# Optimization experiments

Measured on AMD Instinct MI355X. Metric: run time of the kernel, lower is better.

The kernel has to match this reference:

```python
import jax, jax.numpy as jnp
import numpy as np

N_VAR, N_CHK, DV, DC = 8192, 4096, 3, 6
N_EDGE = N_VAR * DV  # == N_CHK * DC = 24576
BATCH = 512
N_ITER = 5
EPS = 1e-12
ATANH_CLIP = 1.0 - 1e-7


def setup_inputs() -> dict:
    # Deterministic (3,6)-regular Tanner graph: each variable has DV edges,
    # each check has DC edges; edge-to-check assignment is a fixed permutation.
    rng = np.random.default_rng(0)
    var_index = np.repeat(np.arange(N_VAR, dtype=np.int32), DV)
    chk_index = rng.permutation(np.repeat(np.arange(N_CHK, dtype=np.int32), DC))
    key = jax.random.key(0)
    llr = jax.random.normal(key, (BATCH, N_VAR), dtype=jnp.float32) * 2.0
    return {
        "llr": llr,
        "var_index": jnp.asarray(var_index, jnp.int32),
        "chk_index": jnp.asarray(chk_index, jnp.int32),
    }


def reference(llr, var_index, chk_index):
    # Messages stored edge-major: [E, batch] so segment ops act on leading axis.
    x = llr.T                              # [N, batch]
    scattered = x[var_index]               # spa.scatter(llr) -> [E, batch]
    ext = jnp.zeros_like(scattered)        # extrinsic_value init
    outs = []
    for _ in range(N_ITER):
        # variable node process: leave-one-out sum of check->var extrinsics
        vsum = jax.ops.segment_sum(ext, var_index, num_segments=N_VAR)
        a_priori = vsum[var_index] - ext   # [E, batch]
        msg = a_priori + scattered
        # check node process: 2*atanh( prod_{e' in check, e'!=e} tanh(msg/2) )
        t = jnp.tanh(msg * 0.5)
        log_abs = jnp.log(jnp.abs(t) + EPS)
        sgn = jnp.sign(t)
        csum_log = jax.ops.segment_sum(log_abs, chk_index, num_segments=N_CHK)
        cprod_sgn = jax.ops.segment_prod(sgn, chk_index, num_segments=N_CHK)
        loo = jnp.exp(csum_log[chk_index] - log_abs) * (cprod_sgn[chk_index] * sgn)
        loo = jnp.clip(loo, -ATANH_CLIP, ATANH_CLIP)
        ext = 2.0 * jnp.arctanh(loo)
        # gather(extrinsic) + llr
        out = jax.ops.segment_sum(ext, var_index, num_segments=N_VAR) + x
        outs.append(out.T)                 # back to [batch, N]
    return jnp.stack(outs)                 # [N_ITER, batch, N]
```

## Files before the change

kernel.cpp:

```cpp
#include <hip/hip_runtime.h>
#include <math.h>

#define N_VAR 8192
#define N_CHK 4096
#define DC 6
#define N_EDGE 24576
#define BATCH 512
#define N_ITER 5
#define CLIP_F 0.99999988f
#define NTHREADS 1024
#define VPT (N_VAR / NTHREADS)
#define CPT (N_CHK / NTHREADS)


__global__ void k_zero(int* __restrict__ cnt) {
    int i = blockIdx.x * blockDim.x + threadIdx.x;
    if (i < N_CHK) cnt[i] = 0;
}

__global__ void k_build(const int* __restrict__ chk_index,
                        int* __restrict__ cnt,
                        int* __restrict__ chk_edges) {
    int e = blockIdx.x * blockDim.x + threadIdx.x;
    if (e < N_EDGE) {
        int c = chk_index[e];
        int p = atomicAdd(&cnt[c], 1);
        chk_edges[c * DC + p] = e;
    }
}

__launch_bounds__(1024, 4)
__global__ void k_spa(const float* __restrict__ llr,
                      const int* __restrict__ chk_edges,
                      float* __restrict__ out) {
    __shared__ float m[N_EDGE];
    const int b = blockIdx.x;
    const int tid = threadIdx.x;
    const float* __restrict__ lrow = llr + (size_t)b * N_VAR;
    float* __restrict__ orow = out + (size_t)b * N_VAR;

    float l[VPT], el[VPT];
    #pragma unroll
    for (int k = 0; k < VPT; ++k) {
        int v = tid + k * NTHREADS;
        l[k]  = lrow[v];
        el[k] = __expf(l[k]);
    }
    int ce[CPT][DC];
    #pragma unroll
    for (int k = 0; k < CPT; ++k) {
        int c = tid + k * NTHREADS;
        #pragma unroll
        for (int j = 0; j < DC; ++j) ce[k][j] = chk_edges[c * DC + j];
    }

    #pragma unroll
    for (int k = 0; k < VPT; ++k) {
        int v = tid + k * NTHREADS;
        float t0 = (el[k] - 1.0f) * __builtin_amdgcn_rcpf(el[k] + 1.0f);
        m[3 * v] = t0; m[3 * v + 1] = t0; m[3 * v + 2] = t0;
    }
    __syncthreads();

    #pragma unroll 1
    for (int iter = 0; iter < N_ITER; ++iter) {
        float tq[CPT][DC];
        #pragma unroll
        for (int k = 0; k < CPT; ++k)
            #pragma unroll
            for (int j = 0; j < DC; ++j) tq[k][j] = m[ce[k][j]];

        #pragma unroll
        for (int k = 0; k < CPT; ++k) {
            float pre[DC + 1], suf[DC + 1];
            pre[0] = 1.0f; suf[DC] = 1.0f;
            #pragma unroll
            for (int j = 0; j < DC; ++j)      pre[j + 1] = pre[j] * tq[k][j];
            #pragma unroll
            for (int j = DC - 1; j >= 0; --j) suf[j] = suf[j + 1] * tq[k][j];
            bool zz = (pre[DC] == 0.0f);
            #pragma unroll
            for (int j = 0; j < DC; ++j) {
                float lo = pre[j] * suf[j + 1];
                lo = fminf(fmaxf(lo, -CLIP_F), CLIP_F);
                float q = (1.0f + lo) * __builtin_amdgcn_rcpf(1.0f - lo);
                tq[k][j] = zz ? 1.0f : q;
            }
        }

        #pragma unroll
        for (int k = 0; k < CPT; ++k)
            #pragma unroll
            for (int j = 0; j < DC; ++j) m[ce[k][j]] = tq[k][j];
        __syncthreads();

        float qv[VPT][3];
        #pragma unroll
        for (int k = 0; k < VPT; ++k) {
            int v = tid + k * NTHREADS;
            qv[k][0] = m[3 * v]; qv[k][1] = m[3 * v + 1]; qv[k][2] = m[3 * v + 2];
        }

        const bool last = (iter == N_ITER - 1);
        #pragma unroll
        for (int k = 0; k < VPT; ++k) {
            int v = tid + k * NTHREADS;
            float q0 = qv[k][0], q1 = qv[k][1], q2 = qv[k][2];
            float q01 = q0 * q1, q12 = q1 * q2, q02 = q0 * q2;
            orow[(size_t)iter * (BATCH * N_VAR) + v] = l[k] + __logf(q01 * q2);
            if (!last) {
                float E0 = el[k] * q12, E1 = el[k] * q02, E2 = el[k] * q01;
                m[3 * v]     = (E0 - 1.0f) * __builtin_amdgcn_rcpf(E0 + 1.0f);
                m[3 * v + 1] = (E1 - 1.0f) * __builtin_amdgcn_rcpf(E1 + 1.0f);
                m[3 * v + 2] = (E2 - 1.0f) * __builtin_amdgcn_rcpf(E2 + 1.0f);
            }
        }
        if (!last) __syncthreads();
    }
}

extern "C" void kernel_launch(void* const* d_in, const int* in_sizes, int n_in,
                              void* d_out, int out_size, void* d_ws, size_t ws_size,
                              hipStream_t stream) {
    const float* llr       = (const float*)d_in[0];
    const int*   chk_index = (const int*)d_in[2];
    float*       out       = (float*)d_out;

    int* cnt       = (int*)d_ws;
    int* chk_edges = cnt + N_CHK;

    k_zero <<<(N_CHK  + 255) / 256, 256, 0, stream>>>(cnt);
    k_build<<<(N_EDGE + 255) / 256, 256, 0, stream>>>(chk_index, cnt, chk_edges);
    k_spa  <<<BATCH, 1024, 0, stream>>>(llr, chk_edges, out);
}
```

Before: 142.8 us.

## Reorder check edges per slot to reduce LDS bank conflicts in gathers

Adds a single-block scheduling kernel that greedily permutes each check's edge list so that, for every slot j, the threads of a wavefront hit different LDS banks (edge index mod 32), aiming to cut bank conflicts in the shared-memory gather and scatter of check messages. It also precomputes byte offsets to save address arithmetic and replaces the zeroing kernel with hipMemsetAsync. The cost is an extra serial-ish setup kernel per call, whose scheduling heuristic groups threads using assumptions about the wavefront mapping.

```diff
diff --git a/kernel.cpp b/kernel.cpp
--- a/kernel.cpp
+++ b/kernel.cpp
@@ -13,11 +13,6 @@
 #define CPT (N_CHK / NTHREADS)
 
 
-__global__ void k_zero(int* __restrict__ cnt) {
-    int i = blockIdx.x * blockDim.x + threadIdx.x;
-    if (i < N_CHK) cnt[i] = 0;
-}
-
 __global__ void k_build(const int* __restrict__ chk_index,
                         int* __restrict__ cnt,
                         int* __restrict__ chk_edges) {
@@ -26,6 +21,46 @@
         int c = chk_index[e];
         int p = atomicAdd(&cnt[c], 1);
         chk_edges[c * DC + p] = e;
+    }
+}
+
+#define NGRP 64
+#define SUBL 8
+#define CPS  8
+
+__global__ __launch_bounds__(512) void k_sched(int* __restrict__ chk_edges) {
+    __shared__ int cnt[NGRP * DC * 33];
+    const int t = threadIdx.x;
+    for (int i = t; i < NGRP * DC * 33; i += 512) cnt[i] = 0;
+    __syncthreads();
+    const int g = t & 63;
+    const int s = t >> 6;
+    const int w = g >> 2, k = g & 3;
+    int* gc = cnt + g * (DC * 33);
+    #pragma unroll 1
+    for (int q = 0; q < CPS; ++q) {
+        int l = s * CPS + q;
+        int c = 64 * w + 1024 * k + l;
+        int E[DC], B[DC];
+        #pragma unroll
+        for (int j = 0; j < DC; ++j) { E[j] = chk_edges[c * DC + j]; B[j] = E[j] & 31; }
+        int used = 0;
+        #pragma unroll
+        for (int j = 0; j < DC; ++j) {
+            int bestC = 0x7fffffff, bestB = 0, bestE = 0, bestI = 0;
+            #pragma unroll
+            for (int i = 0; i < DC; ++i) {
+                int cc = gc[j * 33 + B[i]];
+                bool take = (((used >> i) & 1) == 0) && (cc < bestC);
+                bestC = take ? cc : bestC;
+                bestB = take ? B[i] : bestB;
+                bestE = take ? E[i] : bestE;
+                bestI = take ? i : bestI;
+            }
+            used |= (1 << bestI);
+            atomicAdd(&gc[j * 33 + bestB], 1);
+            chk_edges[c * DC + j] = bestE;
+        }
     }
 }
 
@@ -38,6 +73,7 @@
     const int tid = threadIdx.x;
     const float* __restrict__ lrow = llr + (size_t)b * N_VAR;
     float* __restrict__ orow = out + (size_t)b * N_VAR;
+    char* mb = (char*)m;
 
     float l[VPT], el[VPT];
     #pragma unroll
@@ -46,12 +82,12 @@
         l[k]  = lrow[v];
         el[k] = __expf(l[k]);
     }
-    int ce[CPT][DC];
+    int ceb[CPT][DC];
     #pragma unroll
     for (int k = 0; k < CPT; ++k) {
         int c = tid + k * NTHREADS;
         #pragma unroll
-        for (int j = 0; j < DC; ++j) ce[k][j] = chk_edges[c * DC + j];
+        for (int j = 0; j < DC; ++j) ceb[k][j] = chk_edges[c * DC + j] << 2;
     }
 
     #pragma unroll
@@ -68,7 +104,7 @@
         #pragma unroll
         for (int k = 0; k < CPT; ++k)
             #pragma unroll
-            for (int j = 0; j < DC; ++j) tq[k][j] = m[ce[k][j]];
+            for (int j = 0; j < DC; ++j) tq[k][j] = *(const float*)(mb + ceb[k][j]);
 
         #pragma unroll
         for (int k = 0; k < CPT; ++k) {
@@ -91,7 +127,7 @@
         #pragma unroll
         for (int k = 0; k < CPT; ++k)
             #pragma unroll
-            for (int j = 0; j < DC; ++j) m[ce[k][j]] = tq[k][j];
+            for (int j = 0; j < DC; ++j) *(float*)(mb + ceb[k][j]) = tq[k][j];
         __syncthreads();
 
         float qv[VPT][3];
@@ -129,7 +165,8 @@
     int* cnt       = (int*)d_ws;
     int* chk_edges = cnt + N_CHK;
 
-    k_zero <<<(N_CHK  + 255) / 256, 256, 0, stream>>>(cnt);
+    hipMemsetAsync(cnt, 0, N_CHK * sizeof(int), stream);
     k_build<<<(N_EDGE + 255) / 256, 256, 0, stream>>>(chk_index, cnt, chk_edges);
+    k_sched<<<1, 512, 0, stream>>>(chk_edges);
     k_spa  <<<BATCH, 1024, 0, stream>>>(llr, chk_edges, out);
 }
```

After: 154.1 us. 1.08x slower.
